# Kernel tuning notes

Hardware: AMD Instinct MI355X
Metric: run time of the kernel (lower is better)

Reference implementation:

```python
import jax, jax.numpy as jnp
from jax import lax
import numpy as np

# Static config (see init_kwargs)
D_MODEL = 1024
K = 32          # num_heads
K_Q = 4         # num_query_heads
N_ANCHOR = 4
N_DECAY = K - N_ANCHOR  # 28
M = 8           # num_thetas
KS = 4          # conv kernel size
H = D_MODEL // K  # 32 (expand_factor=1 -> d_inner = d_model)
N_REP = K // K_Q  # 8
DIM_K = D_MODEL
DIM_DECAY = K
DIM_Q = K_Q * H * M * 2  # 2048
TOTAL = DIM_K + DIM_DECAY + DIM_Q  # 3104
B, L = 2, 2048


def setup_inputs() -> dict:
    key = jax.random.key(0)
    ks = jax.random.split(key, 8)
    x = jax.random.normal(ks[0], (B, L, D_MODEL), jnp.float32)
    W_in = jax.random.normal(ks[1], (D_MODEL, TOTAL), jnp.float32) * (D_MODEL ** -0.5)
    # depthwise causal conv kernel: (width, in_per_group=1, channels)
    conv_k = jax.random.normal(ks[2], (KS, 1, DIM_K + DIM_DECAY), jnp.float32) * 0.3
    # theta init (M > 1 branch): linspace(-pi/3, pi/3, M) tiled over (1,1,K,H,M)
    grid = np.linspace(-np.pi / 3, np.pi / 3, M)
    theta = jnp.asarray(np.tile(grid.reshape(1, 1, 1, 1, M), (1, 1, K, H, 1)), jnp.float32)
    decay_slopes = jnp.log(jnp.exp(jnp.asarray(np.geomspace(0.001, 0.1, N_DECAY), jnp.float32)) - 1.0)
    anchor_slopes = jnp.log(jnp.exp(jnp.asarray(np.geomspace(0.01, 0.1, N_ANCHOR), jnp.float32)) - 1.0)
    score_scale = jnp.ones((K,), jnp.float32)
    lim = float(np.sqrt(6.0 / (H + H)))  # glorot uniform
    W_re = jax.random.uniform(ks[3], (H, H), jnp.float32, -lim, lim)
    W_im = jax.random.uniform(ks[4], (H, H), jnp.float32, -lim, lim)
    norm_scale = jnp.ones((2 * H,), jnp.float32)
    W_out = jax.random.normal(ks[5], (D_MODEL, D_MODEL), jnp.float32) * (D_MODEL ** -0.5)
    return dict(x=x, W_in=W_in, conv_k=conv_k, theta=theta, decay_slopes=decay_slopes,
                anchor_slopes=anchor_slopes, score_scale=score_scale, W_re=W_re,
                W_im=W_im, norm_scale=norm_scale, W_out=W_out)


def reference(x, W_in, conv_k, theta, decay_slopes, anchor_slopes, score_scale,
              W_re, W_im, norm_scale, W_out):
    b, l, _ = x.shape
    z = x @ W_in                                    # (b,l,TOTAL)
    z_mem = z[..., :DIM_K + DIM_DECAY]
    q_raw = z[..., DIM_K + DIM_DECAY:]
    # causal depthwise conv over time
    zp = jnp.pad(z_mem, ((0, 0), (KS - 1, 0), (0, 0)))
    z_mem = lax.conv_general_dilated(zp, conv_k, window_strides=(1,), padding='VALID',
                                     dimension_numbers=('NWC', 'WIO', 'NWC'),
                                     feature_group_count=DIM_K + DIM_DECAY)
    k_val = z_mem[..., :DIM_K].reshape(b, l, K, H)
    s_raw = z_mem[..., -K:].reshape(b, l, K, 1)
    q = q_raw.reshape(b, l, K_Q, H, M, 2)
    q_re, q_im = q[..., 0], q[..., 1]
    # ALiBi-like decay / anchor log weights
    pos = jnp.arange(l, dtype=jnp.float32)
    slopes_d = jax.nn.softplus(decay_slopes).reshape(1, 1, N_DECAY, 1)
    dist = jnp.maximum(jnp.float32(l - 1) - pos, 0.0)
    lw_d = -slopes_d * dist[None, :, None, None]        # (1,l,N_DECAY,1)
    slopes_a = jax.nn.softplus(anchor_slopes).reshape(1, 1, N_ANCHOR, 1)
    lw_a = -slopes_a * pos[None, :, None, None]         # (1,l,N_ANCHOR,1)
    log_tw = jnp.concatenate([lw_d, lw_a], axis=2)      # (1,l,K,1)
    log_p = jnp.clip(score_scale[None, None, :, None] * s_raw, -20.0, 20.0)
    p_w = jnp.exp(log_p + log_tw)                       # (b,l,K,1)
    # complex rotary features of keys
    phi = k_val[..., None] * theta                      # (b,l,K,H,M)
    re_k = jnp.cos(phi)
    im_k = jnp.sin(phi)
    # cumulative state
    den = jnp.cumsum(p_w[..., 0], axis=1)               # (b,l,K)
    pwb = p_w[..., None]                                # (b,l,K,1,1)
    num_re = jnp.cumsum(pwb * re_k, axis=1)             # (b,l,K,H,M)
    num_im = jnp.cumsum(pwb * im_k, axis=1)
    inv = lax.rsqrt(jnp.maximum(den, 0.0001))
    inv = (inv * inv)[..., None, None]                  # 1/den, (b,l,K,1,1)
    s_re = (num_re * inv).reshape(b, l, K_Q, N_REP, H, M)
    s_im = (num_im * inv).reshape(b, l, K_Q, N_REP, H, M)
    qr = q_re.reshape(b, l, K_Q, 1, H, M)
    qi = q_im.reshape(b, l, K_Q, 1, H, M)
    out_re = jnp.sum(s_re * qr + s_im * qi, axis=-1).reshape(b, l, K, H)
    out_im = jnp.sum(s_im * qr - s_re * qi, axis=-1).reshape(b, l, K, H)
    # original einsum 'blkh,hh->blkh' uses only the diagonal of W_re / W_im
    y_re = out_re * norm_scale[:H] * jnp.diagonal(W_re)
    y_im = out_im * norm_scale[H:] * jnp.diagonal(W_im)
    y = jax.nn.silu((y_re + y_im).reshape(b, l, DIM_K))
    return y @ W_out
```

## Files before the change

### kernel.cpp

```cpp
#include <hip/hip_runtime.h>
#include <hip/hip_bf16.h>
#include <math.h>

#define D_MODEL   1024
#define K_TOT     32
#define N_DECAY   28
#define M_DIM     8
#define KS        4
#define H_DIM     32
#define DIM_K     1024
#define DIM_MEM   1056
#define DIM_Q     2048
#define TOTAL_DIM 3104
#define NPAD_IN   3328
#define B_SZ      2
#define L_SEQ     2048
#define BL_TOT    4096

#define KG_CNT    4
#define NCHUNK    128
#define CHUNK_L   16

typedef __attribute__((ext_vector_type(8))) __bf16 bf16x8;
typedef __attribute__((ext_vector_type(4))) __bf16 bf16x4;
typedef __attribute__((ext_vector_type(4))) float  f32x4;

__device__ __forceinline__ void gload_lds16(const void* g, void* l) {
    __builtin_amdgcn_global_load_lds(
        (const __attribute__((address_space(1))) void*)g,
        (__attribute__((address_space(3))) void*)l, 16, 0, 0);
}

__global__ __launch_bounds__(512, 2) void gemm_big(const __bf16* __restrict__ A,
                                                   const __bf16* __restrict__ Bt,
                                                   __bf16* __restrict__ Cmem,
                                                   __bf16* __restrict__ Cq,
                                                   int Kdim, int gx) {
    __shared__ __bf16 lds[2][2][256 * 64];

    const int tid  = threadIdx.x;
    const int w    = tid >> 6;
    const int lane = tid & 63;
    const int l15  = lane & 15;
    const int l16  = lane >> 4;
    const int wm   = w >> 2;
    const int wn   = w & 3;

    const int nwg = gridDim.x;
    int lin = blockIdx.x;
    lin = (lin & 7) * (nwg >> 3) + (lin >> 3);
    const int bx = lin % gx, by = lin / gx;
    const int r0 = by * 256, c0 = bx * 256;

    const int srl   = lane >> 3;
    const int sslot = lane & 7;

    f32x4 acc[8][4] = {};
    const int NT = Kdim / 64;

#define STG_A(T, BUF, J)                                                       \
    {                                                                          \
        const int r_  = (J) * 64 + w * 8 + srl;                                \
        const int so_ = sslot ^ (r_ & 7);                                      \
        gload_lds16(A + (size_t)(r0 + r_) * Kdim + (T) * 64 + so_ * 8,         \
                    &lds[BUF][0][((J) * 64 + w * 8) * 64]);                    \
    }
#define STG_B(T, BUF, J)                                                       \
    {                                                                          \
        const int r_  = (J) * 64 + w * 8 + srl;                                \
        const int so_ = sslot ^ (r_ & 7);                                      \
        gload_lds16(Bt + (size_t)(c0 + r_) * Kdim + (T) * 64 + so_ * 8,        \
                    &lds[BUF][1][((J) * 64 + w * 8) * 64]);                    \
    }

#define LOAD_A(AP, MIBASE)                                                     \
    _Pragma("unroll") for (int m2 = 0; m2 < 2; m2++)                           \
        _Pragma("unroll") for (int kk = 0; kk < 2; kk++) {                     \
            const int row_  = wm * 128 + ((MIBASE) + m2) * 16 + l15;           \
            const int slot_ = (kk * 4 + l16) ^ (row_ & 7);                     \
            AP[m2][kk] = *(const bf16x8*)&As_[row_ * 64 + slot_ * 8];          \
        }

#define PHASE(AP, MIBASE)                                                      \
    __builtin_amdgcn_s_barrier();                                              \
    asm volatile("s_waitcnt lgkmcnt(0)" ::: "memory");                         \
    __builtin_amdgcn_sched_barrier(0);                                         \
    __builtin_amdgcn_s_setprio(1);                                             \
    _Pragma("unroll") for (int kk = 0; kk < 2; kk++)                           \
        _Pragma("unroll") for (int m2 = 0; m2 < 2; m2++)                       \
            _Pragma("unroll") for (int ni = 0; ni < 4; ni++)                   \
                acc[(MIBASE) + m2][ni] =                                       \
                    __builtin_amdgcn_mfma_f32_16x16x32_bf16(                   \
                        AP[m2][kk], b[ni][kk], acc[(MIBASE) + m2][ni], 0,0,0); \
    __builtin_amdgcn_s_setprio(0);                                             \
    __builtin_amdgcn_sched_barrier(0);                                         \
    __builtin_amdgcn_s_barrier();

#pragma unroll
    for (int j = 0; j < 4; j++) { STG_A(0, 0, j); STG_B(0, 0, j); }
#pragma unroll
    for (int j = 0; j < 4; j++) { STG_A(1, 1, j); STG_B(1, 1, j); }
    __builtin_amdgcn_sched_barrier(0);
    asm volatile("s_waitcnt vmcnt(8)" ::: "memory");
    __builtin_amdgcn_s_barrier();
    __builtin_amdgcn_sched_barrier(0);

    for (int t = 0; t < NT; ++t) {
        const int cur = t & 1;
        const __bf16* As_ = &lds[cur][0][0];
        const __bf16* Bs_ = &lds[cur][1][0];
        const bool pf = (t + 2 < NT);
        const int tn = t + 2;

        bf16x8 b[4][2], ap[2][2];

#pragma unroll
        for (int ni = 0; ni < 4; ni++)
#pragma unroll
            for (int kk = 0; kk < 2; kk++) {
                const int col  = wn * 64 + ni * 16 + l15;
                const int slot = (kk * 4 + l16) ^ (col & 7);
                b[ni][kk] = *(const bf16x8*)&Bs_[col * 64 + slot * 8];
            }
        LOAD_A(ap, 0);
        PHASE(ap, 0);

        LOAD_A(ap, 2);
        if (pf) { STG_B(tn, cur, 0); STG_B(tn, cur, 1); }
        PHASE(ap, 2);

        LOAD_A(ap, 4);
        if (pf) { STG_B(tn, cur, 2); STG_B(tn, cur, 3);
                  STG_A(tn, cur, 0); STG_A(tn, cur, 2); }
        PHASE(ap, 4);

        LOAD_A(ap, 6);
        PHASE(ap, 6);

        if (pf) { STG_A(tn, cur, 1); STG_A(tn, cur, 3); }
        __builtin_amdgcn_sched_barrier(0);
        if (pf) asm volatile("s_waitcnt vmcnt(8)" ::: "memory");
        else    asm volatile("s_waitcnt vmcnt(0)" ::: "memory");
        __builtin_amdgcn_s_barrier();
        __builtin_amdgcn_sched_barrier(0);
    }
#undef STG_A
#undef STG_B
#undef LOAD_A
#undef PHASE

#pragma unroll
    for (int mi = 0; mi < 8; mi++) {
#pragma unroll
        for (int ni = 0; ni < 4; ni++) {
            const int col = c0 + wn * 64 + ni * 16 + l15;
            const int row = r0 + wm * 128 + mi * 16 + l16 * 4;
            if (col < DIM_MEM) {
#pragma unroll
                for (int q = 0; q < 4; q++)
                    Cmem[(size_t)(row + q) * DIM_MEM + col] = (__bf16)acc[mi][ni][q];
            } else if (col < TOTAL_DIM) {
#pragma unroll
                for (int q = 0; q < 4; q++)
                    Cq[(size_t)(row + q) * DIM_Q + (col - DIM_MEM)] =
                        (__bf16)acc[mi][ni][q];
            }
        }
    }
}

__global__ __launch_bounds__(512, 2) void gemm_mid(const __bf16* __restrict__ A,
                                                   const __bf16* __restrict__ Bt,
                                                   float* __restrict__ C,
                                                   int Ndim, int Kdim, int gx) {
    __shared__ __bf16 lds[2][2][128 * 64];

    const int tid  = threadIdx.x;
    const int w    = tid >> 6;
    const int lane = tid & 63;
    const int l15  = lane & 15;
    const int l16  = lane >> 4;
    const int wm   = w >> 1;
    const int wn   = w & 1;

    const int nwg = gridDim.x;
    int lin = blockIdx.x;
    lin = (lin & 7) * (nwg >> 3) + (lin >> 3);
    const int bx = lin % gx, by = lin / gx;
    const int r0 = by * 128, c0 = bx * 128;

    const int srl   = lane >> 3;
    const int sslot = lane & 7;

    f32x4 acc[2][4] = {};
    const int NT = Kdim / 64;

#define STG4(T, BUF)                                                           \
    _Pragma("unroll") for (int j = 0; j < 2; j++) {                            \
        const int r_  = j * 64 + w * 8 + srl;                                  \
        const int so_ = sslot ^ (r_ & 7);                                      \
        gload_lds16(A + (size_t)(r0 + r_) * Kdim + (T) * 64 + so_ * 8,         \
                    &lds[BUF][0][(j * 64 + w * 8) * 64]);                      \
        gload_lds16(Bt + (size_t)(c0 + r_) * Kdim + (T) * 64 + so_ * 8,        \
                    &lds[BUF][1][(j * 64 + w * 8) * 64]);                      \
    }

    STG4(0, 0);
    STG4(1, 1);
    __builtin_amdgcn_sched_barrier(0);
    asm volatile("s_waitcnt vmcnt(4)" ::: "memory");
    __builtin_amdgcn_s_barrier();
    __builtin_amdgcn_sched_barrier(0);

    for (int t = 0; t < NT; ++t) {
        const int cur = t & 1;
        const __bf16* As_ = &lds[cur][0][0];
        const __bf16* Bs_ = &lds[cur][1][0];
        const bool pf = (t + 2 < NT);

        bf16x8 b[4][2], a[2][2];
#pragma unroll
        for (int ni = 0; ni < 4; ni++)
#pragma unroll
            for (int kk = 0; kk < 2; kk++) {
                const int col  = wn * 64 + ni * 16 + l15;
                const int slot = (kk * 4 + l16) ^ (col & 7);
                b[ni][kk] = *(const bf16x8*)&Bs_[col * 64 + slot * 8];
            }
#pragma unroll
        for (int mi = 0; mi < 2; mi++)
#pragma unroll
            for (int kk = 0; kk < 2; kk++) {
                const int row  = wm * 32 + mi * 16 + l15;
                const int slot = (kk * 4 + l16) ^ (row & 7);
                a[mi][kk] = *(const bf16x8*)&As_[row * 64 + slot * 8];
            }
        asm volatile("s_waitcnt lgkmcnt(0)" ::: "memory");
        __builtin_amdgcn_sched_barrier(0);
        __builtin_amdgcn_s_setprio(1);
#pragma unroll
        for (int kk = 0; kk < 2; kk++)
#pragma unroll
            for (int mi = 0; mi < 2; mi++)
#pragma unroll
                for (int ni = 0; ni < 4; ni++)
                    acc[mi][ni] = __builtin_amdgcn_mfma_f32_16x16x32_bf16(
                        a[mi][kk], b[ni][kk], acc[mi][ni], 0, 0, 0);
        __builtin_amdgcn_s_setprio(0);
        __builtin_amdgcn_sched_barrier(0);
        __builtin_amdgcn_s_barrier();
        if (pf) STG4(t + 2, cur);
        __builtin_amdgcn_sched_barrier(0);
        if (pf) asm volatile("s_waitcnt vmcnt(4)" ::: "memory");
        else    asm volatile("s_waitcnt vmcnt(0)" ::: "memory");
        __builtin_amdgcn_s_barrier();
        __builtin_amdgcn_sched_barrier(0);
    }
#undef STG4

#pragma unroll
    for (int mi = 0; mi < 2; mi++) {
#pragma unroll
        for (int ni = 0; ni < 4; ni++) {
            const int col = c0 + wn * 64 + ni * 16 + l15;
            const int row = r0 + wm * 32 + mi * 16 + l16 * 4;
#pragma unroll
            for (int q = 0; q < 4; q++)
                C[(size_t)(row + q) * Ndim + col] = acc[mi][ni][q];
        }
    }
}

#define CAST_BLOCKS 4096
#define TIN_BX      (NPAD_IN / 32)
#define TIN_BLOCKS  (TIN_BX * (D_MODEL / 32))
#define TOUT_BX     (D_MODEL / 32)
#define TOUT_BLOCKS (TOUT_BX * (D_MODEL / 32))

__global__ __launch_bounds__(256) void prep_all(const float* __restrict__ x,
                                                const float* __restrict__ W_in,
                                                const float* __restrict__ W_out,
                                                __bf16* __restrict__ x_b,
                                                __bf16* __restrict__ W_in_T,
                                                __bf16* __restrict__ W_out_T) {
    __shared__ float tile[32][33];
    const int bid = blockIdx.x;
    const int t = threadIdx.x;

    if (bid < CAST_BLOCKS) {
        const int i = bid * 256 + t;
        const float4 v = ((const float4*)x)[i];
        bf16x4 o;
        o.x = (__bf16)v.x; o.y = (__bf16)v.y; o.z = (__bf16)v.z; o.w = (__bf16)v.w;
        ((bf16x4*)x_b)[i] = o;
        return;
    }

    const bool is_in = (bid < CAST_BLOCKS + TIN_BLOCKS);
    const int lb = is_in ? (bid - CAST_BLOCKS) : (bid - CAST_BLOCKS - TIN_BLOCKS);
    const int bx_ = is_in ? TIN_BX : TOUT_BX;
    const int Ndim = is_in ? TOTAL_DIM : D_MODEL;
    const float* W = is_in ? W_in : W_out;
    __bf16* Wt = is_in ? W_in_T : W_out_T;

    const int n0 = (lb % bx_) * 32, k0 = (lb / bx_) * 32;
    const int tx = t & 31, ty = t >> 5;
#pragma unroll
    for (int i = 0; i < 32; i += 8) {
        float v = 0.f;
        if (n0 + tx < Ndim) v = W[(size_t)(k0 + ty + i) * Ndim + n0 + tx];
        tile[ty + i][tx] = v;
    }
    __syncthreads();
#pragma unroll
    for (int i = 0; i < 32; i += 8) {
        const int n = n0 + ty + i;
        Wt[(size_t)n * D_MODEL + k0 + tx] = (__bf16)tile[tx][ty + i];
    }
}

__global__ __launch_bounds__(256) void conv_pw(const __bf16* __restrict__ z_mem,
                                               const float* __restrict__ conv_k,
                                               const float* __restrict__ score_scale,
                                               const float* __restrict__ decay_slopes,
                                               const float* __restrict__ anchor_slopes,
                                               __bf16* __restrict__ k_val,
                                               float* __restrict__ p_w) {
    const int blk = blockIdx.x;
    const int l0 = (blk << 2) & (L_SEQ - 1);
    const int b  = (blk << 2) >> 11;
    const int t  = threadIdx.x;
    const __bf16* zb = z_mem + (size_t)b * L_SEQ * DIM_MEM;

    {
        const int c = 4 * t;
        float4 ck[KS];
#pragma unroll
        for (int s = 0; s < KS; s++) ck[s] = *(const float4*)&conv_k[s * DIM_MEM + c];

        float4 zr[7];
#pragma unroll
        for (int r = 0; r < 7; r++) {
            const int tl = l0 - 3 + r;
            if (tl >= 0) {
                const bf16x4 v = *(const bf16x4*)&zb[(size_t)tl * DIM_MEM + c];
                zr[r] = make_float4((float)v.x, (float)v.y, (float)v.z, (float)v.w);
            } else zr[r] = make_float4(0.f, 0.f, 0.f, 0.f);
        }
#pragma unroll
        for (int i = 0; i < 4; i++) {
            float4 acc = {0.f, 0.f, 0.f, 0.f};
#pragma unroll
            for (int s = 0; s < KS; s++) {
                acc.x = fmaf(ck[s].x, zr[i + s].x, acc.x);
                acc.y = fmaf(ck[s].y, zr[i + s].y, acc.y);
                acc.z = fmaf(ck[s].z, zr[i + s].z, acc.z);
                acc.w = fmaf(ck[s].w, zr[i + s].w, acc.w);
            }
            bf16x4 o;
            o.x = (__bf16)acc.x; o.y = (__bf16)acc.y;
            o.z = (__bf16)acc.z; o.w = (__bf16)acc.w;
            *(bf16x4*)&k_val[(size_t)(b * L_SEQ + l0 + i) * DIM_K + c] = o;
        }
    }

    if (t < 8) {
        const int c = DIM_K + 4 * t;
        float4 ck[KS];
#pragma unroll
        for (int s = 0; s < KS; s++) ck[s] = *(const float4*)&conv_k[s * DIM_MEM + c];
        float4 zr[7];
#pragma unroll
        for (int r = 0; r < 7; r++) {
            const int tl = l0 - 3 + r;
            if (tl >= 0) {
                const bf16x4 v = *(const bf16x4*)&zb[(size_t)tl * DIM_MEM + c];
                zr[r] = make_float4((float)v.x, (float)v.y, (float)v.z, (float)v.w);
            } else zr[r] = make_float4(0.f, 0.f, 0.f, 0.f);
        }
        float sl[4], lt0[4], lt1[4];
#pragma unroll
        for (int j = 0; j < 4; j++) {
            const int k = 4 * t + j;
            sl[j] = score_scale[k];
            if (k < N_DECAY) {
                const float sd = log1pf(__expf(decay_slopes[k]));
                lt0[j] = -sd * (float)(L_SEQ - 1); lt1[j] = sd;
            } else {
                const float sa = log1pf(__expf(anchor_slopes[k - N_DECAY]));
                lt0[j] = 0.f; lt1[j] = -sa;
            }
        }
#pragma unroll
        for (int i = 0; i < 4; i++) {
            float4 acc = {0.f, 0.f, 0.f, 0.f};
#pragma unroll
            for (int s = 0; s < KS; s++) {
                acc.x = fmaf(ck[s].x, zr[i + s].x, acc.x);
                acc.y = fmaf(ck[s].y, zr[i + s].y, acc.y);
                acc.z = fmaf(ck[s].z, zr[i + s].z, acc.z);
                acc.w = fmaf(ck[s].w, zr[i + s].w, acc.w);
            }
            const float av[4] = {acc.x, acc.y, acc.z, acc.w};
            const int l = l0 + i;
#pragma unroll
            for (int j = 0; j < 4; j++) {
                const float lp = fminf(fmaxf(sl[j] * av[j], -20.f), 20.f);
                p_w[(size_t)(b * L_SEQ + l) * K_TOT + 4 * t + j] =
                    __expf(lp + lt0[j] + lt1[j] * (float)l);
            }
        }
    }
}

__global__ __launch_bounds__(256) void chunk_sums(const __bf16* __restrict__ k_val,
                                                  const float* __restrict__ p_w,
                                                  const float* __restrict__ theta,
                                                  float* __restrict__ csum,
                                                  float* __restrict__ cden) {
    const int idx = blockIdx.x;
    const int c = idx & (NCHUNK - 1);
    const int bkg = idx >> 7;
    const int kg = bkg & (KG_CNT - 1);
    const int b = bkg / KG_CNT;
    const int t = threadIdx.x;
    const int kl = t >> 5;
    const int h = t & 31;
    const int k = kg * 8 + kl;
    const int bk = b * K_TOT + k;

    const float A4 = theta[4];

    float r[4] = {}, im[4] = {};
    float den = 0.f;
    const int l0 = c * CHUNK_L;
#pragma unroll 2
    for (int i = 0; i < CHUNK_L; i++) {
        const size_t bl = (size_t)b * L_SEQ + (l0 + i);
        const float p  = p_w[bl * K_TOT + k];
        const float kv = (float)k_val[bl * DIM_K + k * H_DIM + h];
        float cc = __cosf(kv * A4), ss = __sinf(kv * A4);
        const float cd = fmaf(cc, cc, -(ss * ss));
        const float sd = 2.f * cc * ss;
        r[0]  = fmaf(p, cc, r[0]);
        im[0] = fmaf(p, ss, im[0]);
#pragma unroll
        for (int j = 1; j < 4; j++) {
            const float c2 = fmaf(cc, cd, -(ss * sd));
            ss = fmaf(ss, cd, cc * sd);
            cc = c2;
            r[j]  = fmaf(p, cc, r[j]);
            im[j] = fmaf(p, ss, im[j]);
        }
        den += p;
    }

    float* base = &csum[((size_t)bk * NCHUNK + c) * 256 + h * 8];
    *(f32x4*)base       = f32x4{ r[0], im[0], r[1], im[1] };
    *(f32x4*)(base + 4) = f32x4{ r[2], im[2], r[3], im[3] };
    if (h == 0) cden[bk * NCHUNK + c] = den;
}

__global__ __launch_bounds__(256) void chunk_prefix(float* __restrict__ csum,
                                                    float* __restrict__ cden) {
    const int bk = blockIdx.x;
    const int t = threadIdx.x;
    __shared__ float s_tot;

    float v = 0.f, orig = 0.f;
    if (t < NCHUNK) {
        orig = cden[bk * NCHUNK + t];
        v = orig;
#pragma unroll
        for (int d = 1; d < 64; d <<= 1) {
            const float u = __shfl_up(v, d);
            if ((t & 63) >= d) v += u;
        }
        if (t == 63) s_tot = v;
    }
    __syncthreads();
    if (t < NCHUNK) {
        const float off0 = (t >= 64) ? s_tot : 0.f;
        cden[bk * NCHUNK + t] = v + off0 - orig;
    }

    float run = 0.f;
    for (int g = 0; g < NCHUNK / 8; g++) {
        float vv[8];
#pragma unroll
        for (int j = 0; j < 8; j++)
            vv[j] = csum[((size_t)bk * NCHUNK + g * 8 + j) * 256 + t];
#pragma unroll
        for (int j = 0; j < 8; j++) {
            const float x = vv[j];
            vv[j] = run;
            run += x;
        }
#pragma unroll
        for (int j = 0; j < 8; j++)
            csum[((size_t)bk * NCHUNK + g * 8 + j) * 256 + t] = vv[j];
    }
}

__global__ __launch_bounds__(256) void scan_out(const __bf16* __restrict__ q_b,
                                                const __bf16* __restrict__ k_val,
                                                const float* __restrict__ p_w,
                                                const float* __restrict__ theta,
                                                const float* __restrict__ csum,
                                                const float* __restrict__ cden,
                                                const float* __restrict__ W_re,
                                                const float* __restrict__ W_im,
                                                const float* __restrict__ norm_scale,
                                                __bf16* __restrict__ y) {
    const int idx = blockIdx.x;
    const int c = idx & (NCHUNK - 1);
    const int bkg = idx >> 7;
    const int kg = bkg & (KG_CNT - 1);
    const int b = bkg / KG_CNT;
    const int t = threadIdx.x;
    const int kl = t >> 5;
    const int h = t & 31;
    const int k = kg * 8 + kl;
    const int bk = b * K_TOT + k;

    const float A4 = theta[4];

    float r[4], im[4];
    {
        const float* base = &csum[((size_t)bk * NCHUNK + c) * 256 + h * 8];
        const f32x4 v0 = *(const f32x4*)base;
        const f32x4 v1 = *(const f32x4*)(base + 4);
        r[0] = v0.x; im[0] = v0.y; r[1] = v0.z; im[1] = v0.w;
        r[2] = v1.x; im[2] = v1.y; r[3] = v1.z; im[3] = v1.w;
    }
    float den = cden[bk * NCHUNK + c];

    const float wsc_re = norm_scale[h] * W_re[h * H_DIM + h];
    const float wsc_im = norm_scale[H_DIM + h] * W_im[h * H_DIM + h];

    const int l0 = c * CHUNK_L;
    for (int i = 0; i < CHUNK_L; i++) {
        const size_t bl = (size_t)b * L_SEQ + (l0 + i);
        const float p  = p_w[bl * K_TOT + k];
        const float kv = (float)k_val[bl * DIM_K + k * H_DIM + h];

        const __bf16* qp = &q_b[bl * DIM_Q + (size_t)(kg * H_DIM + h) * 16];
        const bf16x8 q0 = *(const bf16x8*)qp;
        const bf16x8 q1 = *(const bf16x8*)(qp + 8);

        float cc = __cosf(kv * A4), ss = __sinf(kv * A4);
        const float cd = fmaf(cc, cc, -(ss * ss));
        const float sd = 2.f * cc * ss;

        float ore = 0.f, oim = 0.f;
#pragma unroll
        for (int j = 0; j < 4; j++) {
            if (j > 0) {
                const float c2 = fmaf(cc, cd, -(ss * sd));
                ss = fmaf(ss, cd, cc * sd);
                cc = c2;
            }
            r[j]  = fmaf(p, cc, r[j]);
            im[j] = fmaf(p, ss, im[j]);
            const float qrm = (float)q1[2 * j];
            const float qim = (float)q1[2 * j + 1];
            const float qrj = (float)q0[2 * (3 - j)];
            const float qij = (float)q0[2 * (3 - j) + 1];
            ore = fmaf(r[j],  qrm + qrj, fmaf(im[j], qim - qij, ore));
            oim = fmaf(im[j], qrm - qrj, fmaf(-r[j], qim + qij, oim));
        }
        den += p;
        const float inv = __builtin_amdgcn_rcpf(fmaxf(den, 1e-4f));

        const float v = (ore * wsc_re + oim * wsc_im) * inv;
        const float yv = v * __builtin_amdgcn_rcpf(1.0f + __expf(-v));
        y[bl * DIM_K + k * H_DIM + h] = (__bf16)yv;
    }
}

extern "C" void kernel_launch(void* const* d_in, const int* in_sizes, int n_in,
                              void* d_out, int out_size, void* d_ws, size_t ws_size,
                              hipStream_t stream) {
    const float* x            = (const float*)d_in[0];
    const float* W_in         = (const float*)d_in[1];
    const float* conv_k       = (const float*)d_in[2];
    const float* theta        = (const float*)d_in[3];
    const float* decay_slopes = (const float*)d_in[4];
    const float* anchor_slopes= (const float*)d_in[5];
    const float* score_scale  = (const float*)d_in[6];
    const float* W_re         = (const float*)d_in[7];
    const float* W_im         = (const float*)d_in[8];
    const float* norm_scale   = (const float*)d_in[9];
    const float* W_out        = (const float*)d_in[10];
    float* out = (float*)d_out;

    float* ws = (float*)d_ws;
    size_t off = 0;
    float* p_w    = ws + off; off += (size_t)BL_TOT * K_TOT;
    float* csum   = ws + off; off += (size_t)B_SZ * K_TOT * NCHUNK * 256;
    float* cden   = ws + off; off += (size_t)B_SZ * K_TOT * NCHUNK;
    __bf16* z_mem_b = (__bf16*)(ws + off); off += (size_t)BL_TOT * DIM_MEM / 2 + 8;
    __bf16* k_val   = (__bf16*)(ws + off); off += (size_t)BL_TOT * DIM_K / 2;
    __bf16* x_b     = (__bf16*)(ws + off); off += (size_t)BL_TOT * D_MODEL / 2;
    __bf16* W_in_T  = (__bf16*)(ws + off); off += (size_t)NPAD_IN * D_MODEL / 2;
    __bf16* W_out_T = (__bf16*)(ws + off); off += (size_t)D_MODEL * D_MODEL / 2;
    __bf16* y_b     = (__bf16*)(ws + off); off += (size_t)BL_TOT * DIM_K / 2;
    __bf16* q_b     = (__bf16*)(ws + off); off += (size_t)BL_TOT * DIM_Q / 2;

    prep_all<<<CAST_BLOCKS + TIN_BLOCKS + TOUT_BLOCKS, 256, 0, stream>>>(
        x, W_in, W_out, x_b, W_in_T, W_out_T);

    gemm_big<<<(NPAD_IN / 256) * (BL_TOT / 256), 512, 0, stream>>>(
        x_b, W_in_T, z_mem_b, q_b, D_MODEL, NPAD_IN / 256);

    conv_pw<<<BL_TOT / 4, 256, 0, stream>>>(z_mem_b, conv_k, score_scale,
                                            decay_slopes, anchor_slopes, k_val, p_w);
    chunk_sums<<<B_SZ * KG_CNT * NCHUNK, 256, 0, stream>>>(k_val, p_w, theta, csum, cden);
    chunk_prefix<<<B_SZ * K_TOT, 256, 0, stream>>>(csum, cden);
    scan_out<<<B_SZ * KG_CNT * NCHUNK, 256, 0, stream>>>(q_b, k_val, p_w, theta, csum,
                                                         cden, W_re, W_im, norm_scale, y_b);
    gemm_mid<<<(D_MODEL / 128) * (BL_TOT / 128), 512, 0, stream>>>(
        y_b, W_out_T, out, D_MODEL, D_MODEL, D_MODEL / 128);
}
```

Measured before the change: 111.6 us.

## Shrink input GEMM tile to 128x256 with single-buffered LDS and no prefetch

The first GEMM now uses 128-row tiles instead of 256, which doubles the grid, and drops the double-buffered, phase-interleaved prefetch pipeline. It uses a simple load, sync, compute, sync loop with a single LDS buffer. Launch bounds rise to 4 blocks per SM so more workgroups can stay resident and hide latency through occupancy rather than software pipelining. The risks are exposed global-load latency each k-step and less operand reuse per tile.

After: 111.8 us. No clear change (+0.2%).

```diff
diff --git a/kernel.cpp b/kernel.cpp
--- a/kernel.cpp
+++ b/kernel.cpp
@@ -31,12 +31,13 @@
         (__attribute__((address_space(3))) void*)l, 16, 0, 0);
 }
 
-__global__ __launch_bounds__(512, 2) void gemm_big(const __bf16* __restrict__ A,
+__global__ __launch_bounds__(512, 4) void gemm_big(const __bf16* __restrict__ A,
                                                    const __bf16* __restrict__ Bt,
                                                    __bf16* __restrict__ Cmem,
                                                    __bf16* __restrict__ Cq,
                                                    int Kdim, int gx) {
-    __shared__ __bf16 lds[2][2][256 * 64];
+    __shared__ __bf16 As[128 * 64];
+    __shared__ __bf16 Bs[256 * 64];
 
     const int tid  = threadIdx.x;
     const int w    = tid >> 6;
@@ -50,111 +51,65 @@
     int lin = blockIdx.x;
     lin = (lin & 7) * (nwg >> 3) + (lin >> 3);
     const int bx = lin % gx, by = lin / gx;
-    const int r0 = by * 256, c0 = bx * 256;
+    const int r0 = by * 128, c0 = bx * 256;
 
     const int srl   = lane >> 3;
     const int sslot = lane & 7;
 
-    f32x4 acc[8][4] = {};
+    f32x4 acc[4][4] = {};
     const int NT = Kdim / 64;
 
-#define STG_A(T, BUF, J)                                                       \
-    {                                                                          \
-        const int r_  = (J) * 64 + w * 8 + srl;                                \
-        const int so_ = sslot ^ (r_ & 7);                                      \
-        gload_lds16(A + (size_t)(r0 + r_) * Kdim + (T) * 64 + so_ * 8,         \
-                    &lds[BUF][0][((J) * 64 + w * 8) * 64]);                    \
-    }
-#define STG_B(T, BUF, J)                                                       \
-    {                                                                          \
-        const int r_  = (J) * 64 + w * 8 + srl;                                \
-        const int so_ = sslot ^ (r_ & 7);                                      \
-        gload_lds16(Bt + (size_t)(c0 + r_) * Kdim + (T) * 64 + so_ * 8,        \
-                    &lds[BUF][1][((J) * 64 + w * 8) * 64]);                    \
-    }
-
-#define LOAD_A(AP, MIBASE)                                                     \
-    _Pragma("unroll") for (int m2 = 0; m2 < 2; m2++)                           \
-        _Pragma("unroll") for (int kk = 0; kk < 2; kk++) {                     \
-            const int row_  = wm * 128 + ((MIBASE) + m2) * 16 + l15;           \
-            const int slot_ = (kk * 4 + l16) ^ (row_ & 7);                     \
-            AP[m2][kk] = *(const bf16x8*)&As_[row_ * 64 + slot_ * 8];          \
-        }
-
-#define PHASE(AP, MIBASE)                                                      \
-    __builtin_amdgcn_s_barrier();                                              \
-    asm volatile("s_waitcnt lgkmcnt(0)" ::: "memory");                         \
-    __builtin_amdgcn_sched_barrier(0);                                         \
-    __builtin_amdgcn_s_setprio(1);                                             \
-    _Pragma("unroll") for (int kk = 0; kk < 2; kk++)                           \
-        _Pragma("unroll") for (int m2 = 0; m2 < 2; m2++)                       \
-            _Pragma("unroll") for (int ni = 0; ni < 4; ni++)                   \
-                acc[(MIBASE) + m2][ni] =                                       \
-                    __builtin_amdgcn_mfma_f32_16x16x32_bf16(                   \
-                        AP[m2][kk], b[ni][kk], acc[(MIBASE) + m2][ni], 0,0,0); \
-    __builtin_amdgcn_s_setprio(0);                                             \
-    __builtin_amdgcn_sched_barrier(0);                                         \
-    __builtin_amdgcn_s_barrier();
-
-#pragma unroll
-    for (int j = 0; j < 4; j++) { STG_A(0, 0, j); STG_B(0, 0, j); }
-#pragma unroll
-    for (int j = 0; j < 4; j++) { STG_A(1, 1, j); STG_B(1, 1, j); }
-    __builtin_amdgcn_sched_barrier(0);
-    asm volatile("s_waitcnt vmcnt(8)" ::: "memory");
-    __builtin_amdgcn_s_barrier();
-    __builtin_amdgcn_sched_barrier(0);
-
     for (int t = 0; t < NT; ++t) {
-        const int cur = t & 1;
-        const __bf16* As_ = &lds[cur][0][0];
-        const __bf16* Bs_ = &lds[cur][1][0];
-        const bool pf = (t + 2 < NT);
-        const int tn = t + 2;
-
-        bf16x8 b[4][2], ap[2][2];
-
-#pragma unroll
-        for (int ni = 0; ni < 4; ni++)
-#pragma unroll
-            for (int kk = 0; kk < 2; kk++) {
+        const int k0 = t * 64;
+#pragma unroll
+        for (int j = 0; j < 2; j++) {
+            const int r_  = j * 64 + w * 8 + srl;
+            const int so_ = sslot ^ (r_ & 7);
+            gload_lds16(A + (size_t)(r0 + r_) * Kdim + k0 + so_ * 8,
+                        &As[(j * 64 + w * 8) * 64]);
+        }
+#pragma unroll
+        for (int j = 0; j < 4; j++) {
+            const int r_  = j * 64 + w * 8 + srl;
+            const int so_ = sslot ^ (r_ & 7);
+            gload_lds16(Bt + (size_t)(c0 + r_) * Kdim + k0 + so_ * 8,
+                        &Bs[(j * 64 + w * 8) * 64]);
+        }
+        __syncthreads();
+
+#pragma unroll
+        for (int kk = 0; kk < 2; kk++) {
+            bf16x8 a[4], b[4];
+#pragma unroll
+            for (int ni = 0; ni < 4; ni++) {
                 const int col  = wn * 64 + ni * 16 + l15;
                 const int slot = (kk * 4 + l16) ^ (col & 7);
-                b[ni][kk] = *(const bf16x8*)&Bs_[col * 64 + slot * 8];
-            }
-        LOAD_A(ap, 0);
-        PHASE(ap, 0);
-
-        LOAD_A(ap, 2);
-        if (pf) { STG_B(tn, cur, 0); STG_B(tn, cur, 1); }
-        PHASE(ap, 2);
-
-        LOAD_A(ap, 4);
-        if (pf) { STG_B(tn, cur, 2); STG_B(tn, cur, 3);
-                  STG_A(tn, cur, 0); STG_A(tn, cur, 2); }
-        PHASE(ap, 4);
-
-        LOAD_A(ap, 6);
-        PHASE(ap, 6);
-
-        if (pf) { STG_A(tn, cur, 1); STG_A(tn, cur, 3); }
-        __builtin_amdgcn_sched_barrier(0);
-        if (pf) asm volatile("s_waitcnt vmcnt(8)" ::: "memory");
-        else    asm volatile("s_waitcnt vmcnt(0)" ::: "memory");
-        __builtin_amdgcn_s_barrier();
-        __builtin_amdgcn_sched_barrier(0);
-    }
-#undef STG_A
-#undef STG_B
-#undef LOAD_A
-#undef PHASE
-
-#pragma unroll
-    for (int mi = 0; mi < 8; mi++) {
+                b[ni] = *(const bf16x8*)&Bs[col * 64 + slot * 8];
+            }
+#pragma unroll
+            for (int mi = 0; mi < 4; mi++) {
+                const int row  = wm * 64 + mi * 16 + l15;
+                const int slot = (kk * 4 + l16) ^ (row & 7);
+                a[mi] = *(const bf16x8*)&As[row * 64 + slot * 8];
+            }
+            __builtin_amdgcn_s_setprio(1);
+#pragma unroll
+            for (int mi = 0; mi < 4; mi++)
+#pragma unroll
+                for (int ni = 0; ni < 4; ni++)
+                    acc[mi][ni] = __builtin_amdgcn_mfma_f32_16x16x32_bf16(
+                        a[mi], b[ni], acc[mi][ni], 0, 0, 0);
+            __builtin_amdgcn_s_setprio(0);
+        }
+        __syncthreads();
+    }
+
+#pragma unroll
+    for (int mi = 0; mi < 4; mi++) {
 #pragma unroll
         for (int ni = 0; ni < 4; ni++) {
             const int col = c0 + wn * 64 + ni * 16 + l15;
-            const int row = r0 + wm * 128 + mi * 16 + l16 * 4;
+            const int row = r0 + wm * 64 + mi * 16 + l16 * 4;
             if (col < DIM_MEM) {
 #pragma unroll
                 for (int q = 0; q < 4; q++)
@@ -610,7 +565,7 @@
     prep_all<<<CAST_BLOCKS + TIN_BLOCKS + TOUT_BLOCKS, 256, 0, stream>>>(
         x, W_in, W_out, x_b, W_in_T, W_out_T);
 
-    gemm_big<<<(NPAD_IN / 256) * (BL_TOT / 256), 512, 0, stream>>>(
+    gemm_big<<<(NPAD_IN / 256) * (BL_TOT / 128), 512, 0, stream>>>(
         x_b, W_in_T, z_mem_b, q_b, D_MODEL, NPAD_IN / 256);
 
     conv_pw<<<BL_TOT / 4, 256, 0, stream>>>(z_mem_b, conv_k, score_scale,
```
